# Kernel tuning notes

Hardware: AMD Instinct MI355X
Metric: run time of the kernel (lower is better)

Reference implementation:

```python
import math
import jax, jax.numpy as jnp
import numpy as np

B, S, D, H = 2, 2048, 1024, 16
HD = D // H  # 64


def setup_inputs() -> dict:
    key = jax.random.key(0)
    k = jax.random.split(key, 8)
    x = jax.random.normal(k[0], (B, S, D), dtype=jnp.float32)
    # RoPE tables: inv_freq over half dim, emb = concat(freqs, freqs)
    inv_freq = 1.0 / (10000.0 ** (jnp.arange(0, HD, 2, dtype=jnp.float32) / HD))
    pos = jnp.arange(S, dtype=jnp.float32)
    freqs = pos[:, None] * inv_freq[None, :]            # [S, HD/2]
    emb = jnp.concatenate([freqs, freqs], axis=-1)      # [S, HD]
    cos = jnp.cos(emb)[:, None, :]                      # [S, 1, HD] broadcasts over [B,S,H,HD]
    sin = jnp.sin(emb)[:, None, :]
    # causal additive mask [1, 1, S, S]
    neg = jnp.finfo(jnp.float32).min
    mask = jnp.where(jnp.tril(jnp.ones((S, S), dtype=bool)), 0.0, neg)[None, None]
    scale = 0.02
    wq = jax.random.normal(k[1], (D, D), dtype=jnp.float32) * scale
    wk = jax.random.normal(k[2], (D, D), dtype=jnp.float32) * scale
    wv = jax.random.normal(k[3], (D, D), dtype=jnp.float32) * scale
    wo = jax.random.normal(k[4], (D, D), dtype=jnp.float32) * scale
    return {"x": x, "cos": cos, "sin": sin, "mask": mask,
            "wq": wq, "wk": wk, "wv": wv, "wo": wo}


def rotate_half(t):
    t1, t2 = t[..., : t.shape[-1] // 2], t[..., t.shape[-1] // 2:]
    return jnp.concatenate([-t2, t1], axis=-1)


def reference(x, cos, sin, mask, wq, wk, wv, wo):
    b, s, d = x.shape
    # torch nn.Linear: y = x @ W^T  (W is [out, in])
    q = (x @ wq.T).reshape(b, s, H, HD)
    kk = (x @ wk.T).reshape(b, s, H, HD)
    v = (x @ wv.T).reshape(b, s, H, HD)
    q = q * cos + rotate_half(q) * sin
    kk = kk * cos + rotate_half(kk) * sin
    q = q.transpose(0, 2, 1, 3)   # [b, h, s, hd]
    kk = kk.transpose(0, 2, 1, 3)
    v = v.transpose(0, 2, 1, 3)
    scores = jnp.einsum('bhqd,bhkd->bhqk', q, kk) / math.sqrt(HD)
    scores = scores + mask
    probs = jax.nn.softmax(scores.astype(jnp.float32), axis=-1).astype(q.dtype)
    out = jnp.einsum('bhqk,bhkd->bhqd', probs, v)
    out = out.transpose(0, 2, 1, 3).reshape(b, s, d)
    return out @ wo.T
```

## Files before the change

kernel.cpp:

```cpp
#include <hip/hip_runtime.h>
#include <hip/hip_bf16.h>

typedef __hip_bfloat16 bf16;
typedef unsigned short u16;
typedef __attribute__((ext_vector_type(8))) short short8;
typedef __attribute__((ext_vector_type(4))) float floatx4;

constexpr int B_ = 2, S_ = 2048, D_ = 1024, H_ = 16, HD_ = 64;
constexpr int KT = 64, PAD = 72;
constexpr int GK = 1024, BK = 64;

__device__ inline float b2f(u16 u) {
    union { unsigned int i; float f; } v; v.i = ((unsigned int)u) << 16; return v.f;
}
__device__ inline u16 f2b(float f) {
    bf16 h = __float2bfloat16(f); return *(u16*)&h;
}

__device__ inline void gl16(const u16* g, u16* l) {
    __builtin_amdgcn_global_load_lds(
        (const __attribute__((address_space(1))) unsigned int*)g,
        (__attribute__((address_space(3))) unsigned int*)l, 16, 0, 0);
}

#define SBAR() __builtin_amdgcn_sched_barrier(0)

__global__ __launch_bounds__(256) void cvt_kernel(
    const float* __restrict__ x,  const float* __restrict__ wq,
    const float* __restrict__ wk, const float* __restrict__ wv,
    const float* __restrict__ wo,
    u16* __restrict__ Xb, u16* __restrict__ Wb)
{
    const size_t c = (size_t)blockIdx.x * 256 + threadIdx.x;
    const float* src; u16* dst; size_t off;
    if (c < (size_t)(1 << 19)) { src = x; dst = Xb; off = c; }
    else {
        const size_t w = c - (1 << 19);
        const int wi = (int)(w >> 17);
        off = w & ((1 << 17) - 1);
        src = (wi == 0) ? wq : (wi == 1) ? wk : (wi == 2) ? wv : wo;
        dst = Wb + ((size_t)wi << 20);
    }
    const float4 a = *(const float4*)(src + off * 8);
    const float4 b = *(const float4*)(src + off * 8 + 4);
    ushort4 u0; u0.x = f2b(a.x); u0.y = f2b(a.y); u0.z = f2b(a.z); u0.w = f2b(a.w);
    ushort4 u1; u1.x = f2b(b.x); u1.y = f2b(b.y); u1.z = f2b(b.z); u1.w = f2b(b.w);
    *(ushort4*)(dst + off * 8)     = u0;
    *(ushort4*)(dst + off * 8 + 4) = u1;
}

__global__ __launch_bounds__(512, 2) void qkv8(
    const u16* __restrict__ Ag, const u16* __restrict__ Wall,
    const float* __restrict__ cosp, const float* __restrict__ sinp,
    bf16* __restrict__ Qo, bf16* __restrict__ Ko, u16* __restrict__ Vt)
{
    extern __shared__ u16 lds[];

    const int wgid = (blockIdx.x & 7) * 24 + (blockIdx.x >> 3);
    const int mt = wgid / 12;
    const int rem = wgid - mt * 12;
    const int nt = rem & 3, z = rem >> 2;

    const u16* W = Wall + ((size_t)z << 20);
    const int m0 = mt * 256, n0 = nt * 256;

    const int tid  = threadIdx.x;
    const int wave = tid >> 6, lane = tid & 63;
    const int quad = lane >> 4, l16 = lane & 15;
    const int wm = wave >> 2, wn = wave & 3;

    const int lr_st = wave * 16 + (lane >> 2);
    const int csrc  = ((lane & 3) ^ ((lane >> 5) << 1)) * 8;
    const int grA   = ((lr_st >> 6) << 7) + (lr_st & 63);
    const int grB   = ((lr_st >> 5) << 6) + (lr_st & 31);

    const int cidx = ((quad ^ (((l16 >> 3) & 1) << 1))) * 8;

    floatx4 acc[8][4] = {};
    short8 af[4][2], bA[2][2], bB[2][2];

    const u16* A_st = Ag + (size_t)(m0 + grA) * GK + csrc;
    const u16* B_st = W  + (size_t)(n0 + grB) * GK + csrc;

    auto stA = [&](int t2, int mh) {
        if (t2 > 15) return;
        const u16* s = A_st + ((size_t)mh * 64) * GK + t2 * 64;
        u16* d = lds + (((t2 & 1) * 2 + mh) * 8192) + wave * 512;
        gl16(s, d);
        gl16(s + 32, d + 4096);
    };
    auto stB = [&](int t2, int nh) {
        if (t2 > 15) return;
        const u16* s = B_st + ((size_t)nh * 32) * GK + t2 * 64;
        u16* d = lds + 32768 + (((t2 & 1) * 2 + nh) * 8192) + wave * 512;
        gl16(s, d);
        gl16(s + 32, d + 4096);
    };
    auto rdA = [&](int sl, int mh) {
        const int base = (sl * 2 + mh) * 8192 + cidx;
#pragma unroll
        for (int mf = 0; mf < 4; ++mf) {
            const int lr = wm * 64 + mf * 16 + l16;
#pragma unroll
            for (int ks = 0; ks < 2; ++ks)
                af[mf][ks] = *(const short8*)&lds[base + ks * 4096 + lr * 32];
        }
    };
    auto rdB = [&](short8 (&bf)[2][2], int sl, int nh) {
        const int base = 32768 + (sl * 2 + nh) * 8192 + cidx;
#pragma unroll
        for (int fn = 0; fn < 2; ++fn) {
            const int lr = wn * 32 + fn * 16 + l16;
#pragma unroll
            for (int ks = 0; ks < 2; ++ks)
                bf[fn][ks] = *(const short8*)&lds[base + ks * 4096 + lr * 32];
        }
    };
    auto mm = [&](int mh, int nh, short8 (&bf)[2][2]) {
#pragma unroll
        for (int mf = 0; mf < 4; ++mf)
#pragma unroll
            for (int fn = 0; fn < 2; ++fn)
#pragma unroll
                for (int ks = 0; ks < 2; ++ks)
                    acc[mh * 4 + mf][nh * 2 + fn] =
                        __builtin_amdgcn_mfma_f32_16x16x32_bf16(
                            af[mf][ks], bf[fn][ks],
                            acc[mh * 4 + mf][nh * 2 + fn], 0, 0, 0);
    };

    stA(0, 0); stB(0, 0); stA(0, 1); stB(0, 1); stA(1, 0); stB(1, 0);
    asm volatile("s_waitcnt vmcnt(4)" ::: "memory");
    SBAR(); __builtin_amdgcn_s_barrier(); SBAR();

    for (int t = 0; t < 16; ++t) {
        const int sl = t & 1;
        rdA(sl, 0); rdB(bA, sl, 0); stA(t + 1, 1);
        SBAR(); __builtin_amdgcn_s_barrier();
        asm volatile("s_waitcnt lgkmcnt(0)" ::: "memory"); SBAR();
        __builtin_amdgcn_s_setprio(1);
        mm(0, 0, bA);
        __builtin_amdgcn_s_setprio(0);
        SBAR(); __builtin_amdgcn_s_barrier(); SBAR();
        rdB(bB, sl, 1); stB(t + 1, 1);
        SBAR(); __builtin_amdgcn_s_barrier();
        asm volatile("s_waitcnt lgkmcnt(0)" ::: "memory"); SBAR();
        __builtin_amdgcn_s_setprio(1);
        mm(0, 1, bB);
        __builtin_amdgcn_s_setprio(0);
        SBAR(); __builtin_amdgcn_s_barrier(); SBAR();
        rdA(sl, 1); stA(t + 2, 0);
        SBAR(); __builtin_amdgcn_s_barrier();
        asm volatile("s_waitcnt lgkmcnt(0)" ::: "memory"); SBAR();
        __builtin_amdgcn_s_setprio(1);
        mm(1, 0, bA);
        __builtin_amdgcn_s_setprio(0);
        SBAR(); __builtin_amdgcn_s_barrier(); SBAR();
        stB(t + 2, 0);
        SBAR(); __builtin_amdgcn_s_barrier();
        asm volatile("s_waitcnt lgkmcnt(0)" ::: "memory"); SBAR();
        __builtin_amdgcn_s_setprio(1);
        mm(1, 1, bB);
        __builtin_amdgcn_s_setprio(0);
        SBAR();
        if (t < 14)       asm volatile("s_waitcnt vmcnt(4)" ::: "memory");
        else if (t == 14) asm volatile("s_waitcnt vmcnt(0)" ::: "memory");
        SBAR(); __builtin_amdgcn_s_barrier(); SBAR();
    }

    const int s0 = m0 & (S_ - 1);
    const int bq = m0 >> 11;
    const int h  = (n0 >> 6) + wn;

    if (z < 2) {
        float* Cs = (float*)lds;
        float* Sn = (float*)(lds + 16384);
        {
            const int rr = tid >> 1;
            const int cc = (tid & 1) * 16;
            const float4* cp = (const float4*)(cosp + (size_t)(s0 + rr) * HD_ + cc);
            const float4* sp = (const float4*)(sinp + (size_t)(s0 + rr) * HD_ + cc);
            float4* cd = (float4*)&Cs[rr * 32 + cc];
            float4* sd = (float4*)&Sn[rr * 32 + cc];
            cd[0] = cp[0]; cd[1] = cp[1]; cd[2] = cp[2]; cd[3] = cp[3];
            sd[0] = sp[0]; sd[1] = sp[1]; sd[2] = sp[2]; sd[3] = sp[3];
        }
        __syncthreads();

        const float scale = (z == 0) ? 0.125f * 1.44269504f : 1.0f;
        bf16* C = (z == 0) ? Qo : Ko;
#pragma unroll
        for (int mf = 0; mf < 8; ++mf)
#pragma unroll
            for (int r = 0; r < 4; ++r) {
                const int mr = wm * 128 + mf * 16 + quad * 4 + r;
                const size_t base = ((size_t)(bq * H_ + h) * S_ + s0 + mr) << 6;
#pragma unroll
                for (int np = 0; np < 2; ++np) {
                    const int d = np * 16 + l16;
                    const float c1 = Cs[mr * 32 + d];
                    const float s1 = Sn[mr * 32 + d];
                    const float q0 = acc[mf][np][r], q1 = acc[mf][np + 2][r];
                    C[base + d]      = __float2bfloat16((q0 * c1 - q1 * s1) * scale);
                    C[base + d + 32] = __float2bfloat16((q1 * c1 + q0 * s1) * scale);
                }
            }
    } else {
        const int bh = bq * H_ + h;
#pragma unroll
        for (int mf = 0; mf < 8; ++mf)
#pragma unroll
            for (int nf = 0; nf < 4; ++nf) {
                const int hd = nf * 16 + l16;
                const int sb = s0 + wm * 128 + mf * 16 + quad * 4;
                ushort4 pk;
                pk.x = f2b(acc[mf][nf][0]); pk.y = f2b(acc[mf][nf][1]);
                pk.z = f2b(acc[mf][nf][2]); pk.w = f2b(acc[mf][nf][3]);
                *(ushort4*)&Vt[((size_t)(bh * HD_ + hd) << 11) + sb] = pk;
            }
    }
}

template <typename TC, int SCATTER, int ROPE, int BN>
__global__ __launch_bounds__(256) void gemm_async(
    const u16* __restrict__ A, const u16* __restrict__ Wb,
    const float* __restrict__ cosp, const float* __restrict__ sinp,
    TC* __restrict__ C0, TC* __restrict__ C1, TC* __restrict__ C2, int N)
{
    constexpr int NT = BN / 32;

    int x, y, z;
    {
        const int xcd = blockIdx.x & 7, idx = blockIdx.x >> 3;
        y = (xcd & 3) * 8 + (idx & 7);
        if (BN == 128) {
            const int xz = (xcd >> 2) * 12 + (idx >> 3);
            x = xz & 7; z = xz >> 3;
        } else {
            x = (xcd >> 2) * 8 + (idx >> 3);
            z = 0;
        }
    }

    const u16* W = Wb + ((size_t)z << 20);
    TC*        C = (z == 0) ? C0 : (z == 1 ? C1 : C2);

    __shared__ __align__(16) u16 As[128 * BK];
    __shared__ __align__(16) u16 Bs[BN * BK];

    const int tid  = threadIdx.x;
    const int wave = tid >> 6, lane = tid & 63;
    const int quad = lane >> 4, l16 = lane & 15;
    const int wm = wave >> 1, wn = wave & 1;
    const int m0 = y * 128, n0 = x * BN;

    const int srl = lane >> 3;
    const int sc  = (lane & 7) ^ srl;

    floatx4 acc[4][NT] = {};

    for (int k0 = 0; k0 < GK; k0 += BK) {
        __syncthreads();
#pragma unroll
        for (int j = 0; j < 4; ++j) {
            const int rb = wave * 32 + j * 8;
            gl16(A + (size_t)(m0 + rb + srl) * GK + k0 + sc * 8, &As[rb * BK]);
        }
#pragma unroll
        for (int j = 0; j < BN / 32; ++j) {
            const int rb = wave * (BN / 4) + j * 8;
            gl16(W + (size_t)(n0 + rb + srl) * GK + k0 + sc * 8, &Bs[rb * BK]);
        }
        __syncthreads();

#pragma unroll
        for (int ks = 0; ks < 2; ++ks) {
            short8 af[4], bfr[NT];
#pragma unroll
            for (int mt = 0; mt < 4; ++mt) {
                const int R = wm * 64 + mt * 16 + l16;
                af[mt] = *(const short8*)&As[R * BK + (((ks * 4 + quad) ^ (l16 & 7)) * 8)];
            }
#pragma unroll
            for (int nt = 0; nt < NT; ++nt) {
                const int R = wn * (BN / 2) + nt * 16 + l16;
                bfr[nt] = *(const short8*)&Bs[R * BK + (((ks * 4 + quad) ^ (l16 & 7)) * 8)];
            }
#pragma unroll
            for (int mt = 0; mt < 4; ++mt)
#pragma unroll
                for (int nt = 0; nt < NT; ++nt)
                    acc[mt][nt] = __builtin_amdgcn_mfma_f32_16x16x32_bf16(
                        af[mt], bfr[nt], acc[mt][nt], 0, 0, 0);
        }
    }

    {
#pragma unroll
        for (int mt = 0; mt < 4; ++mt)
#pragma unroll
            for (int nt = 0; nt < NT; ++nt)
#pragma unroll
                for (int r = 0; r < 4; ++r) {
                    const int m = m0 + wm * 64 + mt * 16 + quad * 4 + r;
                    const int n = n0 + wn * (BN / 2) + nt * 16 + l16;
                    ((float*)C)[(size_t)m * N + n] = acc[mt][nt][r];
                }
    }
}

__global__ __launch_bounds__(256, 2) void fa_kernel(
    const u16* __restrict__ Qg, const u16* __restrict__ Kg, const u16* __restrict__ Vt,
    bf16* __restrict__ Og)
{
    __shared__ __align__(16) u16 Kt[2][KT * PAD];
    __shared__ __align__(16) u16 Vs[2][KT * PAD];

    const int flat = blockIdx.x;
    const int bh = flat & 31;
    const int qt = (S_ / 128 - 1) - (flat >> 5);
    const int b  = bh >> 4, h = bh & 15;
    const int tid  = threadIdx.x;
    const int wave = tid >> 6, lane = tid & 63;
    const int quad = lane >> 4, l16 = lane & 15;
    const int srow = tid >> 2;
    const int sc4  = tid & 3;
    const int scol = sc4 * 16;
    const int vwb  = (sc4 >> 1) * 32 + (sc4 & 1) * 4;

    const int Q0 = qt * 128;
    const int qrow0 = Q0 + wave * 32;

    union S8U { short8 v; ushort4 q[2]; };

    short8 aq[2][2];
#pragma unroll
    for (int qh = 0; qh < 2; ++qh) {
        const u16* qrow = Qg + ((size_t)bh * S_ + qrow0 + qh * 16 + l16) * HD_;
        aq[qh][0] = *(const short8*)(qrow + quad * 8);
        aq[qh][1] = *(const short8*)(qrow + 32 + quad * 8);
    }

    floatx4 oacc[2][4] = {};
    float lsum[2] = {0.f, 0.f};

    const int T = 2 * qt + 2;

    {
        const u16* kp = Kg + ((size_t)bh * S_ + srow) * HD_ + scol;
        *(short8*)&Kt[0][srow * PAD + scol]     = *(const short8*)kp;
        *(short8*)&Kt[0][srow * PAD + scol + 8] = *(const short8*)(kp + 8);
        const u16* vp = Vt + ((size_t)bh * HD_ + srow) * S_ + scol;
        S8U v0, v1; v0.v = *(const short8*)vp; v1.v = *(const short8*)(vp + 8);
        *(ushort4*)&Vs[0][srow * PAD + vwb]      = v0.q[0];
        *(ushort4*)&Vs[0][srow * PAD + vwb + 8]  = v0.q[1];
        *(ushort4*)&Vs[0][srow * PAD + vwb + 16] = v1.q[0];
        *(ushort4*)&Vs[0][srow * PAD + vwb + 24] = v1.q[1];
    }
    __syncthreads();

    for (int it = 0; it < T; ++it) {
        const int  cur = it & 1;
        const bool pf  = (it + 1 < T);
        const int  kb  = it * KT;
        short8 nk0, nk1; S8U nv0, nv1;
        if (pf) {
            const int kb2 = kb + KT;
            const u16* kp = Kg + ((size_t)bh * S_ + kb2 + srow) * HD_ + scol;
            nk0 = *(const short8*)kp; nk1 = *(const short8*)(kp + 8);
            const u16* vp = Vt + ((size_t)bh * HD_ + srow) * S_ + kb2 + scol;
            nv0.v = *(const short8*)vp; nv1.v = *(const short8*)(vp + 8);
        }

        if (kb <= qrow0 + 31) {
            floatx4 s0[4] = {{0,0,0,0},{0,0,0,0},{0,0,0,0},{0,0,0,0}};
            floatx4 s1[4] = {{0,0,0,0},{0,0,0,0},{0,0,0,0},{0,0,0,0}};
#pragma unroll
            for (int kt = 0; kt < 4; ++kt) {
                const short8 bk0 = *(const short8*)&Kt[cur][(kt * 16 + l16) * PAD + quad * 8];
                const short8 bk1 = *(const short8*)&Kt[cur][(kt * 16 + l16) * PAD + 32 + quad * 8];
                s0[kt] = __builtin_amdgcn_mfma_f32_16x16x32_bf16(bk0, aq[0][0], s0[kt], 0, 0, 0);
                s0[kt] = __builtin_amdgcn_mfma_f32_16x16x32_bf16(bk1, aq[0][1], s0[kt], 0, 0, 0);
                s1[kt] = __builtin_amdgcn_mfma_f32_16x16x32_bf16(bk0, aq[1][0], s1[kt], 0, 0, 0);
                s1[kt] = __builtin_amdgcn_mfma_f32_16x16x32_bf16(bk1, aq[1][1], s1[kt], 0, 0, 0);
            }

            if (kb + 32 >= qrow0) {
                const int t0 = l16 - (kb - qrow0) - quad * 4;
#pragma unroll
                for (int kt = 0; kt < 4; ++kt)
#pragma unroll
                    for (int r = 0; r < 4; ++r) {
                        if (kt * 16 + r > t0)      s0[kt][r] = -1.0e38f;
                        if (kt * 16 + r > t0 + 16) s1[kt][r] = -1.0e38f;
                    }
            }

            short8 a0h0, a0h1, a1h0, a1h1;
            float rs0 = 0.f, rs1 = 0.f;
#pragma unroll
            for (int kt = 0; kt < 4; ++kt)
#pragma unroll
                for (int r = 0; r < 4; ++r) {
                    const float e0 = __builtin_amdgcn_exp2f(s0[kt][r]);
                    const float e1 = __builtin_amdgcn_exp2f(s1[kt][r]);
                    rs0 += e0; rs1 += e1;
                    const int idx = (kt & 1) * 4 + r;
                    if (kt < 2) { a0h0[idx] = (short)f2b(e0); a1h0[idx] = (short)f2b(e1); }
                    else        { a0h1[idx] = (short)f2b(e0); a1h1[idx] = (short)f2b(e1); }
                }
            rs0 += __shfl_xor(rs0, 16); rs0 += __shfl_xor(rs0, 32);
            rs1 += __shfl_xor(rs1, 16); rs1 += __shfl_xor(rs1, 32);
            lsum[0] += rs0; lsum[1] += rs1;

#pragma unroll
            for (int dt = 0; dt < 4; ++dt) {
                const short8 bv0 = *(const short8*)&Vs[cur][(dt * 16 + l16) * PAD + quad * 8];
                const short8 bv1 = *(const short8*)&Vs[cur][(dt * 16 + l16) * PAD + 32 + quad * 8];
                oacc[0][dt] = __builtin_amdgcn_mfma_f32_16x16x32_bf16(bv0, a0h0, oacc[0][dt], 0, 0, 0);
                oacc[0][dt] = __builtin_amdgcn_mfma_f32_16x16x32_bf16(bv1, a0h1, oacc[0][dt], 0, 0, 0);
                oacc[1][dt] = __builtin_amdgcn_mfma_f32_16x16x32_bf16(bv0, a1h0, oacc[1][dt], 0, 0, 0);
                oacc[1][dt] = __builtin_amdgcn_mfma_f32_16x16x32_bf16(bv1, a1h1, oacc[1][dt], 0, 0, 0);
            }
        }

        if (pf) {
            const int nb = cur ^ 1;
            *(short8*)&Kt[nb][srow * PAD + scol]     = nk0;
            *(short8*)&Kt[nb][srow * PAD + scol + 8] = nk1;
            *(ushort4*)&Vs[nb][srow * PAD + vwb]      = nv0.q[0];
            *(ushort4*)&Vs[nb][srow * PAD + vwb + 8]  = nv0.q[1];
            *(ushort4*)&Vs[nb][srow * PAD + vwb + 16] = nv1.q[0];
            *(ushort4*)&Vs[nb][srow * PAD + vwb + 24] = nv1.q[1];
        }
        __syncthreads();
    }

#pragma unroll
    for (int qh = 0; qh < 2; ++qh) {
        const float inv = 1.0f / lsum[qh];
        bf16* orow = Og + ((size_t)(b * S_ + qrow0 + qh * 16 + l16)) * D_ + h * HD_;
#pragma unroll
        for (int dt = 0; dt < 4; ++dt) {
            ushort4 pk;
            pk.x = f2b(oacc[qh][dt][0] * inv);
            pk.y = f2b(oacc[qh][dt][1] * inv);
            pk.z = f2b(oacc[qh][dt][2] * inv);
            pk.w = f2b(oacc[qh][dt][3] * inv);
            *(ushort4*)((u16*)orow + dt * 16 + quad * 4) = pk;
        }
    }
}

extern "C" void kernel_launch(void* const* d_in, const int* in_sizes, int n_in,
                              void* d_out, int out_size, void* d_ws, size_t ws_size,
                              hipStream_t stream)
{
    const float* x    = (const float*)d_in[0];
    const float* cosp = (const float*)d_in[1];
    const float* sinp = (const float*)d_in[2];
    const float* wq   = (const float*)d_in[4];
    const float* wk   = (const float*)d_in[5];
    const float* wv   = (const float*)d_in[6];
    const float* wo   = (const float*)d_in[7];
    float* out = (float*)d_out;

    u16* w0 = (u16*)d_ws;
    const size_t NE = (size_t)B_ * S_ * D_;
    u16* Qb  = w0;
    u16* Kb  = w0 + NE;
    u16* Vtb = w0 + 2 * NE;
    u16* Xb  = w0 + 3 * NE;
    u16* Wb  = w0 + 4 * NE;
    u16* Ab  = Xb;
    u16* Wob = Wb + 3 * (1 << 20);

    static bool inited = false;
    if (!inited) {
        hipFuncSetAttribute((const void*)qkv8,
                            hipFuncAttributeMaxDynamicSharedMemorySize, 131072);
        inited = true;
    }

    cvt_kernel<<<4096, 256, 0, stream>>>(x, wq, wk, wv, wo, Xb, Wb);

    qkv8<<<192, 512, 131072, stream>>>(
        Xb, Wb, cosp, sinp, (bf16*)Qb, (bf16*)Kb, Vtb);

    fa_kernel<<<512, 256, 0, stream>>>(Qb, Kb, Vtb, (bf16*)Ab);

    gemm_async<float, 0, 0, 64><<<512, 256, 0, stream>>>(
        Ab, Wob, cosp, sinp, out, out, out, D_);
}
```

Baseline: 191.1 us.

## Halve flash-attention query tile to 64 rows and balance causal work order

```diff
diff --git a/kernel.cpp b/kernel.cpp
--- a/kernel.cpp
+++ b/kernel.cpp
@@ -309,7 +309,7 @@
     }
 }
 
-__global__ __launch_bounds__(256, 2) void fa_kernel(
+__global__ __launch_bounds__(256, 4) void fa_kernel(
     const u16* __restrict__ Qg, const u16* __restrict__ Kg, const u16* __restrict__ Vt,
     bf16* __restrict__ Og)
 {
@@ -318,7 +318,9 @@
 
     const int flat = blockIdx.x;
     const int bh = flat & 31;
-    const int qt = (S_ / 128 - 1) - (flat >> 5);
+    const int rk = flat >> 5;
+    const int g  = rk >> 3, j = rk & 7;
+    const int qt = (g == 0) ? 31 - j : (g == 1) ? j : (g == 2) ? 23 - j : 8 + j;
     const int b  = bh >> 4, h = bh & 15;
     const int tid  = threadIdx.x;
     const int wave = tid >> 6, lane = tid & 63;
@@ -328,23 +330,21 @@
     const int scol = sc4 * 16;
     const int vwb  = (sc4 >> 1) * 32 + (sc4 & 1) * 4;
 
-    const int Q0 = qt * 128;
-    const int qrow0 = Q0 + wave * 32;
+    const int qrow0 = qt * 64 + wave * 16;
 
     union S8U { short8 v; ushort4 q[2]; };
 
-    short8 aq[2][2];
-#pragma unroll
-    for (int qh = 0; qh < 2; ++qh) {
-        const u16* qrow = Qg + ((size_t)bh * S_ + qrow0 + qh * 16 + l16) * HD_;
-        aq[qh][0] = *(const short8*)(qrow + quad * 8);
-        aq[qh][1] = *(const short8*)(qrow + 32 + quad * 8);
-    }
-
-    floatx4 oacc[2][4] = {};
-    float lsum[2] = {0.f, 0.f};
-
-    const int T = 2 * qt + 2;
+    short8 aq0, aq1;
+    {
+        const u16* qrow = Qg + ((size_t)bh * S_ + qrow0 + l16) * HD_;
+        aq0 = *(const short8*)(qrow + quad * 8);
+        aq1 = *(const short8*)(qrow + 32 + quad * 8);
+    }
+
+    floatx4 oacc[4] = {};
+    float lsum = 0.f;
+
+    const int T = qt + 1;
 
     {
         const u16* kp = Kg + ((size_t)bh * S_ + srow) * HD_ + scol;
@@ -362,67 +362,59 @@
     for (int it = 0; it < T; ++it) {
         const int  cur = it & 1;
         const bool pf  = (it + 1 < T);
-        const int  kb  = it * KT;
         short8 nk0, nk1; S8U nv0, nv1;
         if (pf) {
-            const int kb2 = kb + KT;
+            const int kb2 = (it + 1) * KT;
             const u16* kp = Kg + ((size_t)bh * S_ + kb2 + srow) * HD_ + scol;
             nk0 = *(const short8*)kp; nk1 = *(const short8*)(kp + 8);
             const u16* vp = Vt + ((size_t)bh * HD_ + srow) * S_ + kb2 + scol;
             nv0.v = *(const short8*)vp; nv1.v = *(const short8*)(vp + 8);
         }
 
-        if (kb <= qrow0 + 31) {
-            floatx4 s0[4] = {{0,0,0,0},{0,0,0,0},{0,0,0,0},{0,0,0,0}};
-            floatx4 s1[4] = {{0,0,0,0},{0,0,0,0},{0,0,0,0},{0,0,0,0}};
-#pragma unroll
-            for (int kt = 0; kt < 4; ++kt) {
-                const short8 bk0 = *(const short8*)&Kt[cur][(kt * 16 + l16) * PAD + quad * 8];
-                const short8 bk1 = *(const short8*)&Kt[cur][(kt * 16 + l16) * PAD + 32 + quad * 8];
-                s0[kt] = __builtin_amdgcn_mfma_f32_16x16x32_bf16(bk0, aq[0][0], s0[kt], 0, 0, 0);
-                s0[kt] = __builtin_amdgcn_mfma_f32_16x16x32_bf16(bk1, aq[0][1], s0[kt], 0, 0, 0);
-                s1[kt] = __builtin_amdgcn_mfma_f32_16x16x32_bf16(bk0, aq[1][0], s1[kt], 0, 0, 0);
-                s1[kt] = __builtin_amdgcn_mfma_f32_16x16x32_bf16(bk1, aq[1][1], s1[kt], 0, 0, 0);
+        floatx4 s0[4] = {{0,0,0,0},{0,0,0,0},{0,0,0,0},{0,0,0,0}};
+        __builtin_amdgcn_s_setprio(1);
+#pragma unroll
+        for (int kt = 0; kt < 4; ++kt) {
+            const short8 bk0 = *(const short8*)&Kt[cur][(kt * 16 + l16) * PAD + quad * 8];
+            const short8 bk1 = *(const short8*)&Kt[cur][(kt * 16 + l16) * PAD + 32 + quad * 8];
+            s0[kt] = __builtin_amdgcn_mfma_f32_16x16x32_bf16(bk0, aq0, s0[kt], 0, 0, 0);
+            s0[kt] = __builtin_amdgcn_mfma_f32_16x16x32_bf16(bk1, aq1, s0[kt], 0, 0, 0);
+        }
+        __builtin_amdgcn_s_setprio(0);
+
+        if (it == T - 1) {
+            const int t0 = wave * 16 + l16 - quad * 4;
+#pragma unroll
+            for (int kt = 0; kt < 4; ++kt)
+#pragma unroll
+                for (int r = 0; r < 4; ++r)
+                    if (kt * 16 + r > t0) s0[kt][r] = -1.0e38f;
+        }
+
+        short8 ah0, ah1;
+        float rs = 0.f;
+#pragma unroll
+        for (int kt = 0; kt < 4; ++kt)
+#pragma unroll
+            for (int r = 0; r < 4; ++r) {
+                const float e0 = __builtin_amdgcn_exp2f(s0[kt][r]);
+                rs += e0;
+                const int idx = (kt & 1) * 4 + r;
+                if (kt < 2) ah0[idx] = (short)f2b(e0);
+                else        ah1[idx] = (short)f2b(e0);
             }
-
-            if (kb + 32 >= qrow0) {
-                const int t0 = l16 - (kb - qrow0) - quad * 4;
-#pragma unroll
-                for (int kt = 0; kt < 4; ++kt)
-#pragma unroll
-                    for (int r = 0; r < 4; ++r) {
-                        if (kt * 16 + r > t0)      s0[kt][r] = -1.0e38f;
-                        if (kt * 16 + r > t0 + 16) s1[kt][r] = -1.0e38f;
-                    }
-            }
-
-            short8 a0h0, a0h1, a1h0, a1h1;
-            float rs0 = 0.f, rs1 = 0.f;
-#pragma unroll
-            for (int kt = 0; kt < 4; ++kt)
-#pragma unroll
-                for (int r = 0; r < 4; ++r) {
-                    const float e0 = __builtin_amdgcn_exp2f(s0[kt][r]);
-                    const float e1 = __builtin_amdgcn_exp2f(s1[kt][r]);
-                    rs0 += e0; rs1 += e1;
-                    const int idx = (kt & 1) * 4 + r;
-                    if (kt < 2) { a0h0[idx] = (short)f2b(e0); a1h0[idx] = (short)f2b(e1); }
-                    else        { a0h1[idx] = (short)f2b(e0); a1h1[idx] = (short)f2b(e1); }
-                }
-            rs0 += __shfl_xor(rs0, 16); rs0 += __shfl_xor(rs0, 32);
-            rs1 += __shfl_xor(rs1, 16); rs1 += __shfl_xor(rs1, 32);
-            lsum[0] += rs0; lsum[1] += rs1;
-
-#pragma unroll
-            for (int dt = 0; dt < 4; ++dt) {
-                const short8 bv0 = *(const short8*)&Vs[cur][(dt * 16 + l16) * PAD + quad * 8];
-                const short8 bv1 = *(const short8*)&Vs[cur][(dt * 16 + l16) * PAD + 32 + quad * 8];
-                oacc[0][dt] = __builtin_amdgcn_mfma_f32_16x16x32_bf16(bv0, a0h0, oacc[0][dt], 0, 0, 0);
-                oacc[0][dt] = __builtin_amdgcn_mfma_f32_16x16x32_bf16(bv1, a0h1, oacc[0][dt], 0, 0, 0);
-                oacc[1][dt] = __builtin_amdgcn_mfma_f32_16x16x32_bf16(bv0, a1h0, oacc[1][dt], 0, 0, 0);
-                oacc[1][dt] = __builtin_amdgcn_mfma_f32_16x16x32_bf16(bv1, a1h1, oacc[1][dt], 0, 0, 0);
-            }
-        }
+        rs += __shfl_xor(rs, 16); rs += __shfl_xor(rs, 32);
+        lsum += rs;
+
+        __builtin_amdgcn_s_setprio(1);
+#pragma unroll
+        for (int dt = 0; dt < 4; ++dt) {
+            const short8 bv0 = *(const short8*)&Vs[cur][(dt * 16 + l16) * PAD + quad * 8];
+            const short8 bv1 = *(const short8*)&Vs[cur][(dt * 16 + l16) * PAD + 32 + quad * 8];
+            oacc[dt] = __builtin_amdgcn_mfma_f32_16x16x32_bf16(bv0, ah0, oacc[dt], 0, 0, 0);
+            oacc[dt] = __builtin_amdgcn_mfma_f32_16x16x32_bf16(bv1, ah1, oacc[dt], 0, 0, 0);
+        }
+        __builtin_amdgcn_s_setprio(0);
 
         if (pf) {
             const int nb = cur ^ 1;
@@ -436,19 +428,16 @@
         __syncthreads();
     }
 
-#pragma unroll
-    for (int qh = 0; qh < 2; ++qh) {
-        const float inv = 1.0f / lsum[qh];
-        bf16* orow = Og + ((size_t)(b * S_ + qrow0 + qh * 16 + l16)) * D_ + h * HD_;
-#pragma unroll
-        for (int dt = 0; dt < 4; ++dt) {
-            ushort4 pk;
-            pk.x = f2b(oacc[qh][dt][0] * inv);
-            pk.y = f2b(oacc[qh][dt][1] * inv);
-            pk.z = f2b(oacc[qh][dt][2] * inv);
-            pk.w = f2b(oacc[qh][dt][3] * inv);
-            *(ushort4*)((u16*)orow + dt * 16 + quad * 4) = pk;
-        }
+    const float inv = 1.0f / lsum;
+    bf16* orow = Og + ((size_t)(b * S_ + qrow0 + l16)) * D_ + h * HD_;
+#pragma unroll
+    for (int dt = 0; dt < 4; ++dt) {
+        ushort4 pk;
+        pk.x = f2b(oacc[dt][0] * inv);
+        pk.y = f2b(oacc[dt][1] * inv);
+        pk.z = f2b(oacc[dt][2] * inv);
+        pk.w = f2b(oacc[dt][3] * inv);
+        *(ushort4*)((u16*)orow + dt * 16 + quad * 4) = pk;
     }
 }
 
@@ -487,7 +476,7 @@
     qkv8<<<192, 512, 131072, stream>>>(
         Xb, Wb, cosp, sinp, (bf16*)Qb, (bf16*)Kb, Vtb);
 
-    fa_kernel<<<512, 256, 0, stream>>>(Qb, Kb, Vtb, (bf16*)Ab);
+    fa_kernel<<<1024, 256, 0, stream>>>(Qb, Kb, Vtb, (bf16*)Ab);
 
     gemm_async<float, 0, 0, 64><<<512, 256, 0, stream>>>(
         Ab, Wob, cosp, sinp, out, out, out, D_);
```

Measured after the change: 176.3 us. 7.7% less time.
